# Kernel tuning notes

Measured on AMD Instinct MI355X. Metric: run time of the kernel, lower is better.

## Reference

```python
import jax, jax.numpy as jnp
import numpy as np

NUM_NODE = 8192
N_PTS = 20000
FEAT_DIM = 32
POS_THRESH = 0.1
NEG_THRESH = 1.4
POS_RADIUS = 0.0375   # hardcoded literal in the original forward
NEG_RADIUS = 0.1      # hardcoded literal in the original forward
BIG = 100000.0
EPS = 1e-7


def setup_inputs() -> dict:
    key = jax.random.key(0)
    k1, k2, k3, k4, k5, k6, k7 = jax.random.split(key, 7)
    # points in a small box so pos (<0.0375) and neg (>0.1) masks are both populated
    src_pcd = jax.random.uniform(k1, (N_PTS, 3), dtype=jnp.float32) * 0.2
    tgt_pcd = jax.random.uniform(k2, (N_PTS, 3), dtype=jnp.float32) * 0.2
    src_feats = jax.random.normal(k3, (N_PTS, FEAT_DIM), dtype=jnp.float32)
    tgt_feats = jax.random.normal(k4, (N_PTS, FEAT_DIM), dtype=jnp.float32)
    correspondence = jax.random.randint(k5, (NUM_NODE, 2), 0, N_PTS, dtype=jnp.int64)
    # near-identity rigid transform so transformed src stays in the same scale regime
    rot = jnp.eye(3, dtype=jnp.float32) + 0.01 * jax.random.normal(k6, (3, 3), dtype=jnp.float32)
    trans = 0.01 * jax.random.normal(k7, (3, 1), dtype=jnp.float32)
    return {
        "src_pcd": src_pcd, "tgt_pcd": tgt_pcd,
        "src_feats": src_feats, "tgt_feats": tgt_feats,
        "correspondence": correspondence, "rot": rot, "trans": trans,
    }


def _pdist_l2(A, B):
    # GEMM form of sqrt(sum((a-b)^2) + 1e-7); same math as the broadcasted original
    d2 = (jnp.sum(A * A, axis=1)[:, None]
          + jnp.sum(B * B, axis=1)[None, :]
          - 2.0 * A @ B.T)
    return jnp.sqrt(jnp.maximum(d2, 0.0) + EPS)


def reference(src_pcd, tgt_pcd, src_feats, tgt_feats, correspondence, rot, trans):
    # rigid transform of src cloud: (R @ P^T + t)^T
    src_pcd = (rot @ src_pcd.T + trans).T
    ci = correspondence[:, 0]
    cj = correspondence[:, 1]
    sel_src_pts = src_pcd[ci]       # [N,3]
    sel_tgt_pts = tgt_pcd[cj]       # [N,3]
    sel_src_feats = src_feats[ci]   # [N,D]
    sel_tgt_feats = tgt_feats[cj]   # [N,D]

    pts_dist = _pdist_l2(sel_src_pts, sel_tgt_pts)      # [N,N]
    feats_dist = _pdist_l2(sel_src_feats, sel_tgt_feats)  # [N,N]

    pos_mask = pts_dist < POS_RADIUS
    neg_mask = pts_dist > NEG_RADIUS

    furthest_positive = jnp.max(feats_dist * pos_mask.astype(feats_dist.dtype), axis=-1)
    closest_negative = jnp.min(jnp.where(neg_mask, feats_dist, BIG), axis=-1)

    pos_loss = jax.nn.relu(furthest_positive - POS_THRESH)
    neg_loss = jax.nn.relu(NEG_THRESH - closest_negative)
    loss = pos_loss.mean() + neg_loss.mean()
    return loss
```

## Files before the change

kernel.cpp:

```cpp
#include <hip/hip_runtime.h>
#include <math.h>
#include <float.h>

#define NN 8192

typedef __bf16 bf16x8 __attribute__((ext_vector_type(8)));
typedef float f32x4 __attribute__((ext_vector_type(4)));

constexpr float POS_R2 = 0.0375f * 0.0375f;
constexpr float NEG_R2 = 0.1f * 0.1f;
constexpr float EPSF = 1e-7f;
constexpr float PRC = POS_R2 - EPSF;
constexpr float NRC = NEG_R2 - EPSF;
constexpr float POS_TH = 0.1f;
constexpr float NEG_TH = 1.4f;

#define FT_OFF 0
#define FS2_OFF (NN * 64)
#define PSX_OFF (2 * NN * 64)
#define PTX_OFF (3 * NN * 64)
#define FNS_OFF (4 * NN * 64)
#define FNT_OFF (4 * NN * 64 + NN * 4)
#define MAXB_OFF (4 * NN * 64 + 2 * NN * 4)
#define MINB_OFF (4 * NN * 64 + 3 * NN * 4)

__global__ __launch_bounds__(256) void hcl_prep(
    const float* __restrict__ src_pcd, const float* __restrict__ tgt_pcd,
    const float* __restrict__ src_feats, const float* __restrict__ tgt_feats,
    const int* __restrict__ corr, const float* __restrict__ rot,
    const float* __restrict__ trans, char* __restrict__ ws) {
  int t = blockIdx.x * 256 + threadIdx.x;
  int i = t >> 2;
  int p = t & 3;
  int ci = corr[2 * i];
  int cj = corr[2 * i + 1];

  const float4* sf = (const float4*)(src_feats + (size_t)ci * 32);
  const float4* tf = (const float4*)(tgt_feats + (size_t)cj * 32);
  float na = 0.f, nb = 0.f;
  bf16x8 osrc, otgt;
#pragma unroll
  for (int h = 0; h < 2; ++h) {
    float4 a = sf[2 * p + h];
    __bf16 h0 = (__bf16)a.x, h1 = (__bf16)a.y, h2 = (__bf16)a.z, h3 = (__bf16)a.w;
    float f0 = (float)h0, f1 = (float)h1, f2 = (float)h2, f3 = (float)h3;
    na += f0 * f0 + f1 * f1 + f2 * f2 + f3 * f3;
    osrc[4 * h + 0] = (__bf16)(-2.f * f0);
    osrc[4 * h + 1] = (__bf16)(-2.f * f1);
    osrc[4 * h + 2] = (__bf16)(-2.f * f2);
    osrc[4 * h + 3] = (__bf16)(-2.f * f3);

    float4 b = tf[2 * p + h];
    __bf16 g0 = (__bf16)b.x, g1 = (__bf16)b.y, g2 = (__bf16)b.z, g3 = (__bf16)b.w;
    nb += (float)g0 * (float)g0 + (float)g1 * (float)g1 + (float)g2 * (float)g2 +
          (float)g3 * (float)g3;
    otgt[4 * h + 0] = g0;
    otgt[4 * h + 1] = g1;
    otgt[4 * h + 2] = g2;
    otgt[4 * h + 3] = g3;
  }
  *(bf16x8*)(ws + FS2_OFF + (size_t)i * 64 + p * 16) = osrc;
  *(bf16x8*)(ws + FT_OFF + (size_t)i * 64 + p * 16) = otgt;

  na += __shfl_xor(na, 1, 4);
  na += __shfl_xor(na, 2, 4);
  nb += __shfl_xor(nb, 1, 4);
  nb += __shfl_xor(nb, 2, 4);

  __bf16 one = (__bf16)1.0f, zero = (__bf16)0.0f;

  if (p == 0) {
    ((float*)(ws + FNS_OFF))[i] = na;
    ((float*)(ws + FNT_OFF))[i] = nb;
    ((unsigned int*)(ws + MAXB_OFF))[i] = 0u;
    ((unsigned int*)(ws + MINB_OFF))[i] = 0x7F7FFFFFu;
  } else if (p == 1) {
    float r00 = rot[0], r01 = rot[1], r02 = rot[2];
    float r10 = rot[3], r11 = rot[4], r12 = rot[5];
    float r20 = rot[6], r21 = rot[7], r22 = rot[8];
    float t0 = trans[0], t1 = trans[1], t2 = trans[2];
    float px = src_pcd[ci * 3 + 0], py = src_pcd[ci * 3 + 1], pz = src_pcd[ci * 3 + 2];
    float qx = r00 * px + r01 * py + r02 * pz + t0;
    float qy = r10 * px + r11 * py + r12 * pz + t1;
    float qz = r20 * px + r21 * py + r22 * pz + t2;
    float sa = qx * qx + qy * qy + qz * qz;
    __bf16 qhx = (__bf16)qx, qhy = (__bf16)qy, qhz = (__bf16)qz;
    __bf16 qlx = (__bf16)(qx - (float)qhx);
    __bf16 qly = (__bf16)(qy - (float)qhy);
    __bf16 qlz = (__bf16)(qz - (float)qhz);
    __bf16 sah = (__bf16)sa;
    __bf16 sal = (__bf16)(sa - (float)sah);
    bf16x8 v0, v1, vz;
    v0[0] = qhx; v0[1] = qhy; v0[2] = qhz; v0[3] = qhx; v0[4] = qhy; v0[5] = qhz;
    v0[6] = qlx; v0[7] = qly;
    v1[0] = qlz; v1[1] = sah; v1[2] = sal; v1[3] = one; v1[4] = one;
    v1[5] = zero; v1[6] = zero; v1[7] = zero;
#pragma unroll
    for (int k = 0; k < 8; ++k) vz[k] = zero;
    bf16x8* o = (bf16x8*)(ws + PSX_OFF + (size_t)i * 64);
    o[0] = v0; o[1] = v1; o[2] = vz; o[3] = vz;
  } else if (p == 2) {
    float ux = tgt_pcd[cj * 3 + 0], uy = tgt_pcd[cj * 3 + 1], uz = tgt_pcd[cj * 3 + 2];
    float sb = ux * ux + uy * uy + uz * uz;
    __bf16 uhx = (__bf16)ux, uhy = (__bf16)uy, uhz = (__bf16)uz;
    __bf16 ulx = (__bf16)(ux - (float)uhx);
    __bf16 uly = (__bf16)(uy - (float)uhy);
    __bf16 ulz = (__bf16)(uz - (float)uhz);
    __bf16 sbh = (__bf16)sb;
    __bf16 sbl = (__bf16)(sb - (float)sbh);
    __bf16 m2hx = (__bf16)(-2.f * (float)uhx), m2hy = (__bf16)(-2.f * (float)uhy),
           m2hz = (__bf16)(-2.f * (float)uhz);
    __bf16 m2lx = (__bf16)(-2.f * (float)ulx), m2ly = (__bf16)(-2.f * (float)uly),
           m2lz = (__bf16)(-2.f * (float)ulz);
    bf16x8 w0, w1, wz;
    w0[0] = m2hx; w0[1] = m2hy; w0[2] = m2hz; w0[3] = m2lx; w0[4] = m2ly; w0[5] = m2lz;
    w0[6] = m2hx; w0[7] = m2hy;
    w1[0] = m2hz; w1[1] = one; w1[2] = one; w1[3] = sbh; w1[4] = sbl;
    w1[5] = zero; w1[6] = zero; w1[7] = zero;
#pragma unroll
    for (int k = 0; k < 8; ++k) wz[k] = zero;
    bf16x8* o = (bf16x8*)(ws + PTX_OFF + (size_t)i * 64);
    o[0] = w0; o[1] = w1; o[2] = wz; o[3] = wz;
  }
}

__global__ __launch_bounds__(256, 4) void hcl_dist(char* __restrict__ ws) {
  const int lane = threadIdx.x & 63;
  const int wave = threadIdx.x >> 6;
  const int quad = lane >> 4;
  const int n = lane & 15;
  const int i0 = blockIdx.y * 128 + wave * 32;
  const int j0 = blockIdx.x * 512;
  const size_t aoff = (size_t)quad * 16;
  const bool ldp = quad < 2;

  const bf16x8 afeat0 = *(const bf16x8*)(ws + FS2_OFF + (size_t)(i0 + n) * 64 + aoff);
  const bf16x8 afeat1 = *(const bf16x8*)(ws + FS2_OFF + (size_t)(i0 + 16 + n) * 64 + aoff);
  bf16x8 apos0, apos1;
  if (ldp) {
    apos0 = *(const bf16x8*)(ws + PSX_OFF + (size_t)(i0 + n) * 64 + aoff);
    apos1 = *(const bf16x8*)(ws + PSX_OFF + (size_t)(i0 + 16 + n) * 64 + aoff);
  } else {
#pragma unroll
    for (int k = 0; k < 8; ++k) { apos0[k] = (__bf16)0.0f; apos1[k] = (__bf16)0.0f; }
  }
  const f32x4 fa0 = *(const f32x4*)(ws + FNS_OFF + (size_t)(i0 + quad * 4) * 4);
  const f32x4 fa1 = *(const f32x4*)(ws + FNS_OFF + (size_t)(i0 + 16 + quad * 4) * 4);

  float maxv[8], minv[8];
#pragma unroll
  for (int r = 0; r < 8; ++r) {
    maxv[r] = -1.0f;
    minv[r] = FLT_MAX;
  }

  const char* pF = ws + FT_OFF + (size_t)(j0 + n) * 64 + aoff;
  const char* pP = ws + PTX_OFF + (size_t)(j0 + n) * 64 + aoff;
  const char* pN = ws + FNT_OFF + (size_t)(j0 + n) * 4;

  for (int s = 0; s < 8; ++s) {
#pragma unroll
    for (int u = 0; u < 4; ++u) {
      const bf16x8 bfeat = *(const bf16x8*)(pF + u * 1024);
      bf16x8 bpos;
#pragma unroll
      for (int k = 0; k < 8; ++k) bpos[k] = (__bf16)0.0f;
      if (ldp) bpos = *(const bf16x8*)(pP + u * 1024);
      const float fb = *(const float*)(pN + u * 64);

      f32x4 c0, c1, z;
      c0[0] = fa0[0] + fb; c0[1] = fa0[1] + fb; c0[2] = fa0[2] + fb; c0[3] = fa0[3] + fb;
      c1[0] = fa1[0] + fb; c1[1] = fa1[1] + fb; c1[2] = fa1[2] + fb; c1[3] = fa1[3] + fb;
      z[0] = 0.f; z[1] = 0.f; z[2] = 0.f; z[3] = 0.f;

      f32x4 d0 = __builtin_amdgcn_mfma_f32_16x16x32_bf16(afeat0, bfeat, c0, 0, 0, 0);
      f32x4 d1 = __builtin_amdgcn_mfma_f32_16x16x32_bf16(afeat1, bfeat, c1, 0, 0, 0);
      f32x4 u0 = __builtin_amdgcn_mfma_f32_16x16x32_bf16(apos0, bpos, z, 0, 0, 0);
      f32x4 u1 = __builtin_amdgcn_mfma_f32_16x16x32_bf16(apos1, bpos, z, 0, 0, 0);

#pragma unroll
      for (int r = 0; r < 4; ++r) {
        bool p0 = u0[r] < PRC, g0 = u0[r] > NRC;
        maxv[r] = fmaxf(maxv[r], p0 ? d0[r] : -1.0f);
        minv[r] = fminf(minv[r], g0 ? d0[r] : FLT_MAX);
        bool p1 = u1[r] < PRC, g1 = u1[r] > NRC;
        maxv[4 + r] = fmaxf(maxv[4 + r], p1 ? d1[r] : -1.0f);
        minv[4 + r] = fminf(minv[4 + r], g1 ? d1[r] : FLT_MAX);
      }
    }
    pF += 4096;
    pP += 4096;
    pN += 256;
  }

  unsigned int* maxb = (unsigned int*)(ws + MAXB_OFF);
  unsigned int* minb = (unsigned int*)(ws + MINB_OFF);
#pragma unroll
  for (int r = 0; r < 8; ++r) {
    float mx = maxv[r], mn = minv[r];
#pragma unroll
    for (int sh = 1; sh <= 8; sh <<= 1) {
      mx = fmaxf(mx, __shfl_xor(mx, sh, 64));
      mn = fminf(mn, __shfl_xor(mn, sh, 64));
    }
    if (n == 0) {
      int row = i0 + (r < 4 ? 0 : 16) + quad * 4 + (r & 3);
      atomicMax(maxb + row, __float_as_uint(fmaxf(mx, 0.f)));
      atomicMin(minb + row, __float_as_uint(fmaxf(mn, 0.f)));
    }
  }
}

__global__ __launch_bounds__(256) void hcl_loss(const char* __restrict__ ws,
                                               float* __restrict__ out) {
  int t = threadIdx.x;
  const float4* maxb = (const float4*)(ws + MAXB_OFF);
  const float4* minb = (const float4*)(ws + MINB_OFF);
  float sp = 0.f, sn = 0.f;
#pragma unroll
  for (int k = 0; k < 8; ++k) {
    float4 mx = maxb[t + 256 * k];
    float4 mn = minb[t + 256 * k];
    sp += fmaxf(sqrtf(mx.x + EPSF) - POS_TH, 0.f) + fmaxf(sqrtf(mx.y + EPSF) - POS_TH, 0.f) +
          fmaxf(sqrtf(mx.z + EPSF) - POS_TH, 0.f) + fmaxf(sqrtf(mx.w + EPSF) - POS_TH, 0.f);
    sn += fmaxf(NEG_TH - sqrtf(mn.x + EPSF), 0.f) + fmaxf(NEG_TH - sqrtf(mn.y + EPSF), 0.f) +
          fmaxf(NEG_TH - sqrtf(mn.z + EPSF), 0.f) + fmaxf(NEG_TH - sqrtf(mn.w + EPSF), 0.f);
  }
  __shared__ float red[8];
#pragma unroll
  for (int s = 32; s >= 1; s >>= 1) {
    sp += __shfl_down(sp, s, 64);
    sn += __shfl_down(sn, s, 64);
  }
  int wid = t >> 6;
  if ((t & 63) == 0) {
    red[wid] = sp;
    red[4 + wid] = sn;
  }
  __syncthreads();
  if (t == 0) {
    float tsp = red[0] + red[1] + red[2] + red[3];
    float tsn = red[4] + red[5] + red[6] + red[7];
    out[0] = (tsp + tsn) * (1.0f / NN);
  }
}

extern "C" void kernel_launch(void* const* d_in, const int* in_sizes, int n_in,
                              void* d_out, int out_size, void* d_ws, size_t ws_size,
                              hipStream_t stream) {
  const float* src_pcd = (const float*)d_in[0];
  const float* tgt_pcd = (const float*)d_in[1];
  const float* src_feats = (const float*)d_in[2];
  const float* tgt_feats = (const float*)d_in[3];
  const int* corr = (const int*)d_in[4];
  const float* rot = (const float*)d_in[5];
  const float* trans = (const float*)d_in[6];
  float* out = (float*)d_out;
  char* ws = (char*)d_ws;

  hcl_prep<<<NN * 4 / 256, 256, 0, stream>>>(src_pcd, tgt_pcd, src_feats, tgt_feats, corr,
                                             rot, trans, ws);
  hcl_dist<<<dim3(16, 64), 256, 0, stream>>>(ws);
  hcl_loss<<<1, 256, 0, stream>>>(ws, out);
}
```

Baseline: 101.5 us.

## Stage target tiles in double-buffered swizzled LDS shared across waves

Instead of each wave loading target feature, position and norm fragments straight from global memory, the block cooperatively loads each 64-column chunk into XOR-swizzled shared memory, with register prefetch of the next chunk while computing the current one. All four waves read the same B tile from LDS, which cuts redundant global/L2 traffic by up to fourfold. The cost is two block-wide barriers per chunk and about 12.8KB of LDS per block, which may limit occupancy at the 4-blocks target and add sync stalls.

```diff
diff --git a/kernel.cpp b/kernel.cpp
--- a/kernel.cpp
+++ b/kernel.cpp
@@ -125,8 +125,11 @@
 }
 
 __global__ __launch_bounds__(256, 4) void hcl_dist(char* __restrict__ ws) {
-  const int lane = threadIdx.x & 63;
-  const int wave = threadIdx.x >> 6;
+  __shared__ __align__(16) char smem[2][6400];
+
+  const int t = threadIdx.x;
+  const int lane = t & 63;
+  const int wave = t >> 6;
   const int quad = lane >> 4;
   const int n = lane & 15;
   const int i0 = blockIdx.y * 128 + wave * 32;
@@ -147,6 +150,25 @@
   const f32x4 fa0 = *(const f32x4*)(ws + FNS_OFF + (size_t)(i0 + quad * 4) * 4);
   const f32x4 fa1 = *(const f32x4*)(ws + FNS_OFF + (size_t)(i0 + 16 + quad * 4) * 4);
 
+  const int ftq = (t & 3) ^ ((t >> 3) & 3);
+  const size_t ft_g = FT_OFF + (size_t)(t >> 2) * 64 + ftq * 16;
+  const int pxq = (t & 1) ^ ((t >> 3) & 1);
+  const size_t px_g = PTX_OFF + (size_t)(t >> 1) * 64 + pxq * 16;
+
+  uint4 rft{}, rpx{};
+  float rfn = 0.f;
+
+  {
+    const size_t cb = (size_t)j0 * 64;
+    rft = *(const uint4*)(ws + ft_g + cb);
+    if (t < 128) rpx = *(const uint4*)(ws + px_g + cb);
+    if (t < 64) rfn = *(const float*)(ws + FNT_OFF + (size_t)(j0 + t) * 4);
+    *(uint4*)(smem[0] + t * 16) = rft;
+    if (t < 128) *(uint4*)(smem[0] + 4096 + t * 16) = rpx;
+    if (t < 64) *(float*)(smem[0] + 6144 + t * 4) = rfn;
+  }
+  __syncthreads();
+
   float maxv[8], minv[8];
 #pragma unroll
   for (int r = 0; r < 8; ++r) {
@@ -154,19 +176,28 @@
     minv[r] = FLT_MAX;
   }
 
-  const char* pF = ws + FT_OFF + (size_t)(j0 + n) * 64 + aoff;
-  const char* pP = ws + PTX_OFF + (size_t)(j0 + n) * 64 + aoff;
-  const char* pN = ws + FNT_OFF + (size_t)(j0 + n) * 4;
-
+  const int swF = n * 64 + ((quad ^ ((n >> 1) & 3)) << 4);
+  const int swP = 4096 + n * 32 + ((quad ^ ((n >> 2) & 1)) << 4);
+  const int swN = 6144 + n * 4;
+
+  int cur = 0;
   for (int s = 0; s < 8; ++s) {
+    if (s < 7) {
+      const size_t cb = (size_t)(j0 + (s + 1) * 64) * 64;
+      rft = *(const uint4*)(ws + ft_g + cb);
+      if (t < 128) rpx = *(const uint4*)(ws + px_g + cb);
+      if (t < 64) rfn = *(const float*)(ws + FNT_OFF + (size_t)(j0 + (s + 1) * 64 + t) * 4);
+    }
+
+    const char* sb = smem[cur];
 #pragma unroll
     for (int u = 0; u < 4; ++u) {
-      const bf16x8 bfeat = *(const bf16x8*)(pF + u * 1024);
+      const bf16x8 bfeat = *(const bf16x8*)(sb + u * 1024 + swF);
       bf16x8 bpos;
 #pragma unroll
       for (int k = 0; k < 8; ++k) bpos[k] = (__bf16)0.0f;
-      if (ldp) bpos = *(const bf16x8*)(pP + u * 1024);
-      const float fb = *(const float*)(pN + u * 64);
+      if (ldp) bpos = *(const bf16x8*)(sb + u * 512 + swP);
+      const float fb = *(const float*)(sb + u * 64 + swN);
 
       f32x4 c0, c1, z;
       c0[0] = fa0[0] + fb; c0[1] = fa0[1] + fb; c0[2] = fa0[2] + fb; c0[3] = fa0[3] + fb;
@@ -188,9 +219,16 @@
         minv[4 + r] = fminf(minv[4 + r], g1 ? d1[r] : FLT_MAX);
       }
     }
-    pF += 4096;
-    pP += 4096;
-    pN += 256;
+
+    if (s < 7) {
+      __syncthreads();
+      char* nb = smem[cur ^ 1];
+      *(uint4*)(nb + t * 16) = rft;
+      if (t < 128) *(uint4*)(nb + 4096 + t * 16) = rpx;
+      if (t < 64) *(float*)(nb + 6144 + t * 4) = rfn;
+      __syncthreads();
+      cur ^= 1;
+    }
   }
 
   unsigned int* maxb = (unsigned int*)(ws + MAXB_OFF);
```

Result: no change. 102.2 us (+0.7%).
